# Optimization experiments

Measured on AMD Instinct MI355X. Metric: run time of the kernel, lower is better.

The kernel has to match this reference:

```python
import jax, jax.numpy as jnp
from jax import lax
import numpy as np

B, T, D, H, C = 64, 256, 1024, 1024, 27


def _lstm_layer(x, Wih, Whh, bih, bhh):
    """Batch-first LSTM layer matching torch.nn.LSTM gate math.
    x: (N, S, Din) -> returns hs: (N, S, H). Gate order: i, f, g, o."""
    N = x.shape[0]
    Hh = Whh.shape[1]
    # precompute input contribution for all steps: (N, S, 4H)
    xg = jnp.einsum('nsd,gd->nsg', x, Wih) + bih + bhh

    def step(carry, xg_t):
        h, c = carry
        g = xg_t + h @ Whh.T  # (N, 4H)
        i, f, gg, o = jnp.split(g, 4, axis=-1)
        c = jax.nn.sigmoid(f) * c + jax.nn.sigmoid(i) * jnp.tanh(gg)
        h = jax.nn.sigmoid(o) * jnp.tanh(c)
        return (h, c), h

    h0 = jnp.zeros((N, Hh), x.dtype)
    (_, _), hs = lax.scan(step, (h0, h0), jnp.swapaxes(xg, 0, 1))  # scan over S
    return jnp.swapaxes(hs, 0, 1)  # (N, S, H)


def setup_inputs() -> dict:
    key = jax.random.key(0)
    ks = jax.random.split(key, 13)
    s = 1.0 / np.sqrt(H)
    u = lambda k, shape: jax.random.uniform(k, shape, jnp.float32, -s, s)
    return {
        'x': jax.random.normal(ks[0], (B, T, D), jnp.float32),
        'Wih0': u(ks[1], (4 * H, D)), 'Whh0': u(ks[2], (4 * H, H)),
        'bih0': u(ks[3], (4 * H,)), 'bhh0': u(ks[4], (4 * H,)),
        'Wih1': u(ks[5], (4 * H, H)), 'Whh1': u(ks[6], (4 * H, H)),
        'bih1': u(ks[7], (4 * H,)), 'bhh1': u(ks[8], (4 * H,)),
        'W1': u(ks[9], (H // 2, H)), 'b1': u(ks[10], (H // 2,)),
        'W2': u(ks[11], (C, H // 2)), 'b2': u(ks[12], (C,)),
    }


def reference(x, Wih0, Whh0, bih0, bhh0, Wih1, Whh1, bih1, bhh1, W1, b1, W2, b2):
    # Original module permutes (B,T,D) -> (T,B,D) but the LSTM is batch_first,
    # so it treats T as batch and recurs over the original batch axis B.
    xp = jnp.transpose(x, (1, 0, 2))           # (T, B, D): batch=T, seq=B
    h1 = _lstm_layer(xp, Wih0, Whh0, bih0, bhh0)  # (T, B, H)
    h2 = _lstm_layer(h1, Wih1, Whh1, bih1, bhh1)  # (T, B, H)
    out = h2[-1]                                # (B, H): last 'batch' row
    fc = jax.nn.relu(out @ W1.T + b1)
    return fc @ W2.T + b2                       # (B, C)
```

## Files before the change

kernel.cpp:

```cpp
#include <hip/hip_runtime.h>
#include <math.h>


#define NBLK 256
#define TPB  512
#define HDIM 1024
#define SEQ  64
#define CHAIN (SEQ * HDIM)
#define GUARD (1L << 20)
#define POISON 0xAAAAAAAAu
#define ENCOFF 0x55555555u

#define FMA4(A, W, Hv)                                                         \
  do {                                                                         \
    (A).x = fmaf((W).x, (Hv).x, (A).x);                                        \
    (A).y = fmaf((W).y, (Hv).y, (A).y);                                        \
    (A).z = fmaf((W).z, (Hv).z, (A).z);                                        \
    (A).w = fmaf((W).w, (Hv).w, (A).w);                                        \
  } while (0)

__device__ __forceinline__ float sigmoidf_(float v) {
  return 1.0f / (1.0f + expf(-v));
}
__device__ __forceinline__ float hsum4(float4 a) {
  return (a.x + a.y) + (a.z + a.w);
}
__device__ __forceinline__ float wave_sum(float v) {
#pragma unroll
  for (int m = 32; m >= 1; m >>= 1) v += __shfl_xor(v, m, 64);
  return v;
}

__device__ __forceinline__ void st_u32(unsigned* p, unsigned v) {
  __hip_atomic_store(p, v, __ATOMIC_RELAXED, __HIP_MEMORY_SCOPE_AGENT);
}
__device__ __forceinline__ unsigned enc(float v) {
  return __float_as_uint(v) + ENCOFF;
}
__device__ __forceinline__ float dec(unsigned u) {
  return __uint_as_float(u - ENCOFF);
}
__device__ __forceinline__ float2 poll2(const unsigned* p) {
  const unsigned long long* pp = (const unsigned long long*)p;
  unsigned lo, hi;
  long g = 0;
  for (;;) {
    unsigned long long u =
        __hip_atomic_load(pp, __ATOMIC_RELAXED, __HIP_MEMORY_SCOPE_AGENT);
    lo = (unsigned)u;
    hi = (unsigned)(u >> 32);
    if ((lo != POISON) & (hi != POISON)) break;
    __builtin_amdgcn_s_sleep(1);
    if (++g > GUARD) break;
  }
  asm volatile("" ::: "memory");
  return make_float2(dec(lo), dec(hi));
}

__global__ void __launch_bounds__(TPB, 2) lstm_persist(
    const float* __restrict__ x,
    const float* __restrict__ Wih0, const float* __restrict__ Whh0,
    const float* __restrict__ bih0, const float* __restrict__ bhh0,
    const float* __restrict__ Wih1, const float* __restrict__ Whh1,
    const float* __restrict__ bih1, const float* __restrict__ bhh1,
    const float* __restrict__ W1, const float* __restrict__ b1,
    const float* __restrict__ W2, const float* __restrict__ b2,
    float* __restrict__ out, unsigned* ws, int nrep) {
  __shared__ float sA[2][HDIM];
  __shared__ float sB[2][HDIM];
  __shared__ float sX[2][HDIM];

  unsigned* h1rep = ws;
  unsigned* h2rep = ws + (size_t)nrep * CHAIN;
  unsigned* fcb = ws + 2ull * (size_t)nrep * CHAIN;

  const int tid = threadIdx.x;
  const int b = blockIdx.x;
  const int lane = tid & 63;
  const int q = tid >> 6;
  const int L = q >> 2;
  const int elem = (b << 2) + (q & 3);

  const int rep = b & (nrep - 1);
  unsigned* h1r = h1rep + (size_t)rep * CHAIN;
  unsigned* h2r = h2rep + (size_t)rep * CHAIN;

  const float* Wih = L ? Wih1 : Wih0;
  const float* Whh = L ? Whh1 : Whh0;
  const float* bi = L ? bih1 : bih0;
  const float* bh = L ? bhh1 : bhh0;

  float4 wi[4][4], wr[4][4];
  float bias[4];
#pragma unroll
  for (int g = 0; g < 4; ++g) {
    const int row = (g << 10) + elem;
    bias[g] = bi[row] + bh[row];
    const float4* pi = (const float4*)(Wih + (size_t)row * HDIM);
    const float4* pr = (const float4*)(Whh + (size_t)row * HDIM);
#pragma unroll
    for (int k = 0; k < 4; ++k) {
      wi[g][k] = pi[(k << 6) + lane];
      wr[g][k] = pr[(k << 6) + lane];
    }
  }

  float cell = 0.0f;

  for (int p = 0; p <= SEQ; ++p) {
    const int pb = p & 1;
    float2 xv = make_float2(0, 0);
    if (p < SEQ)
      xv = ((const float2*)x)[(size_t)(p * 256 + 255) * 512 + tid];
    float2 vb = make_float2(0, 0);
    if (p >= 2) vb = poll2(h2r + (size_t)(p - 2) * HDIM + (tid << 1));
    float2 va = make_float2(0, 0);
    if (p >= 1) va = poll2(h1r + (size_t)(p - 1) * HDIM + (tid << 1));

    ((float2*)sA[pb])[tid] = va;
    ((float2*)sB[pb])[tid] = vb;
    ((float2*)sX[pb])[tid] = xv;
    __syncthreads();

    const float4* A4 = (const float4*)sA[pb];
    const float4* B4 = (const float4*)sB[pb];
    const float4* X4 = (const float4*)sX[pb];

    if (L == 0) {
      if (p < SEQ) {
        float4 acc[4];
#pragma unroll
        for (int g = 0; g < 4; ++g) acc[g] = make_float4(0, 0, 0, 0);
#pragma unroll
        for (int k = 0; k < 4; ++k) {
          float4 xf = X4[(k << 6) + lane];
          float4 hf = A4[(k << 6) + lane];
#pragma unroll
          for (int g = 0; g < 4; ++g) {
            FMA4(acc[g], wi[g][k], xf);
            FMA4(acc[g], wr[g][k], hf);
          }
        }
        float gi = wave_sum(hsum4(acc[0])) + bias[0];
        float gf = wave_sum(hsum4(acc[1])) + bias[1];
        float gg = wave_sum(hsum4(acc[2])) + bias[2];
        float go = wave_sum(hsum4(acc[3])) + bias[3];
        cell = sigmoidf_(gf) * cell + sigmoidf_(gi) * tanhf(gg);
        float hv = sigmoidf_(go) * tanhf(cell);
        if (lane < nrep)
          st_u32(h1rep + (size_t)lane * CHAIN + (size_t)p * HDIM + elem,
                 enc(hv));
      }
    } else {
      if (p >= 1) {
        float4 acc[4];
#pragma unroll
        for (int g = 0; g < 4; ++g) acc[g] = make_float4(0, 0, 0, 0);
#pragma unroll
        for (int k = 0; k < 4; ++k) {
          float4 iv = A4[(k << 6) + lane];
          float4 hf = B4[(k << 6) + lane];
#pragma unroll
          for (int g = 0; g < 4; ++g) {
            FMA4(acc[g], wi[g][k], iv);
            FMA4(acc[g], wr[g][k], hf);
          }
        }
        float gi = wave_sum(hsum4(acc[0])) + bias[0];
        float gf = wave_sum(hsum4(acc[1])) + bias[1];
        float gg = wave_sum(hsum4(acc[2])) + bias[2];
        float go = wave_sum(hsum4(acc[3])) + bias[3];
        cell = sigmoidf_(gf) * cell + sigmoidf_(gi) * tanhf(gg);
        float hv = sigmoidf_(go) * tanhf(cell);
        if (lane < nrep)
          st_u32(h2rep + (size_t)lane * CHAIN + (size_t)(p - 1) * HDIM + elem,
                 enc(hv));
      }
    }
  }

  __syncthreads();
  {
    const int s = b >> 2, ch = b & 3;
    float2 v = poll2(h2r + (size_t)s * HDIM + (tid << 1));
    ((float2*)sA[0])[tid] = v;
    __syncthreads();
    const float4* A4 = (const float4*)sA[0];
    for (int t = 0; t < 16; ++t) {
      const int j = (ch << 7) + (q << 4) + t;
      const float4* w4 = (const float4*)(W1 + (size_t)j * HDIM);
      float4 acc = make_float4(0, 0, 0, 0);
#pragma unroll
      for (int k = 0; k < 4; ++k) {
        float4 wv = w4[(k << 6) + lane];
        float4 hv = A4[(k << 6) + lane];
        FMA4(acc, wv, hv);
      }
      float v2 = wave_sum(hsum4(acc));
      if (lane == 0)
        st_u32(fcb + (size_t)s * 512 + j, enc(fmaxf(v2 + b1[j], 0.0f)));
    }
  }

  if (b < 64) {
    if (tid < 256) {
      float2 v = poll2(fcb + (size_t)b * 512 + (tid << 1));
      ((float2*)sB[0])[tid] = v;
    }
    __syncthreads();
    const float4* B4v = (const float4*)sB[0];
    for (int c = q; c < 27; c += 8) {
      const float4* w4 = (const float4*)(W2 + (size_t)c * 512);
      float4 acc = make_float4(0, 0, 0, 0);
#pragma unroll
      for (int k = 0; k < 2; ++k) {
        float4 wv = w4[(k << 6) + lane];
        float4 hv = B4v[(k << 6) + lane];
        FMA4(acc, wv, hv);
      }
      float v = wave_sum(hsum4(acc));
      if (lane == 0) out[b * 27 + c] = v + b2[c];
    }
  }
}

extern "C" void kernel_launch(void* const* d_in, const int* in_sizes, int n_in,
                              void* d_out, int out_size, void* d_ws,
                              size_t ws_size, hipStream_t stream) {
  (void)in_sizes; (void)n_in; (void)out_size;
  const float* x    = (const float*)d_in[0];
  const float* Wih0 = (const float*)d_in[1];
  const float* Whh0 = (const float*)d_in[2];
  const float* bih0 = (const float*)d_in[3];
  const float* bhh0 = (const float*)d_in[4];
  const float* Wih1 = (const float*)d_in[5];
  const float* Whh1 = (const float*)d_in[6];
  const float* bih1 = (const float*)d_in[7];
  const float* bhh1 = (const float*)d_in[8];
  const float* W1   = (const float*)d_in[9];
  const float* b1   = (const float*)d_in[10];
  const float* W2   = (const float*)d_in[11];
  const float* b2   = (const float*)d_in[12];
  float* out = (float*)d_out;
  unsigned* ws = (unsigned*)d_ws;

  int nrep = 1;
  for (int r = 8; r >= 1; r >>= 1) {
    size_t need = (2ull * (size_t)r * CHAIN + (size_t)SEQ * 512) * 4ull;
    if (need <= ws_size) { nrep = r; break; }
  }

  hipLaunchKernelGGL(lstm_persist, dim3(NBLK), dim3(TPB), 0, stream, x, Wih0,
                     Whh0, bih0, bhh0, Wih1, Whh1, bih1, bhh1, W1, b1, W2, b2,
                     out, ws, nrep);
}
```

Baseline: 394.2 us.

## Precompute layer-0 input projection for all steps before the recurrent loop

Layer-0 input gate contributions (Wih0·x + biases) for all 64 timesteps are computed up front in a prologue and kept in shared memory. This removes the per-step x load and the input-matmul FMAs from the layer-0 critical path of the serial recurrence. In exchange it adds a prologue in which each block streams its Wih0 rows and the x rows, and layer-0 warps no longer hold Wih0 in registers.

```diff
diff --git a/kernel.cpp b/kernel.cpp
--- a/kernel.cpp
+++ b/kernel.cpp
@@ -68,7 +68,7 @@
     float* __restrict__ out, unsigned* ws, int nrep) {
   __shared__ float sA[2][HDIM];
   __shared__ float sB[2][HDIM];
-  __shared__ float sX[2][HDIM];
+  __shared__ float xg[16][SEQ];
 
   unsigned* h1rep = ws;
   unsigned* h2rep = ws + (size_t)nrep * CHAIN;
@@ -79,39 +79,62 @@
   const int lane = tid & 63;
   const int q = tid >> 6;
   const int L = q >> 2;
-  const int elem = (b << 2) + (q & 3);
+  const int e = q & 3;
+  const int elem = (b << 2) + e;
 
   const int rep = b & (nrep - 1);
   unsigned* h1r = h1rep + (size_t)rep * CHAIN;
   unsigned* h2r = h2rep + (size_t)rep * CHAIN;
 
-  const float* Wih = L ? Wih1 : Wih0;
-  const float* Whh = L ? Whh1 : Whh0;
-  const float* bi = L ? bih1 : bih0;
-  const float* bh = L ? bhh1 : bhh0;
-
   float4 wi[4][4], wr[4][4];
   float bias[4];
-#pragma unroll
-  for (int g = 0; g < 4; ++g) {
-    const int row = (g << 10) + elem;
-    bias[g] = bi[row] + bh[row];
-    const float4* pi = (const float4*)(Wih + (size_t)row * HDIM);
-    const float4* pr = (const float4*)(Whh + (size_t)row * HDIM);
-#pragma unroll
-    for (int k = 0; k < 4; ++k) {
-      wi[g][k] = pi[(k << 6) + lane];
-      wr[g][k] = pr[(k << 6) + lane];
-    }
-  }
+  if (L == 0) {
+#pragma unroll
+    for (int g = 0; g < 4; ++g) {
+      const int row = (g << 10) + elem;
+      const float4* pr = (const float4*)(Whh0 + (size_t)row * HDIM);
+#pragma unroll
+      for (int k = 0; k < 4; ++k) wr[g][k] = pr[(k << 6) + lane];
+      bias[g] = 0.f;
+    }
+  } else {
+#pragma unroll
+    for (int g = 0; g < 4; ++g) {
+      const int row = (g << 10) + elem;
+      bias[g] = bih1[row] + bhh1[row];
+      const float4* pi = (const float4*)(Wih1 + (size_t)row * HDIM);
+      const float4* pr = (const float4*)(Whh1 + (size_t)row * HDIM);
+#pragma unroll
+      for (int k = 0; k < 4; ++k) {
+        wi[g][k] = pi[(k << 6) + lane];
+        wr[g][k] = pr[(k << 6) + lane];
+      }
+    }
+  }
+
+  for (int r = q; r < 16; r += 8) {
+    const int g = r >> 2, ee = r & 3;
+    const int grow = (g << 10) + (b << 2) + ee;
+    const float4* wrow = (const float4*)(Wih0 + (size_t)grow * HDIM);
+    const float4* xrow =
+        (const float4*)(x + (size_t)(lane * 256 + 255) * HDIM);
+    float4 a0 = make_float4(0.f, 0.f, 0.f, 0.f);
+    float4 a1 = make_float4(0.f, 0.f, 0.f, 0.f);
+#pragma unroll 4
+    for (int kk = 0; kk < 256; kk += 2) {
+      float4 w0 = wrow[kk], x0 = xrow[kk];
+      float4 w1 = wrow[kk + 1], x1 = xrow[kk + 1];
+      FMA4(a0, w0, x0);
+      FMA4(a1, w1, x1);
+    }
+    xg[r][lane] = hsum4(a0) + hsum4(a1) + bih0[grow] + bhh0[grow];
+  }
+  __syncthreads();
 
   float cell = 0.0f;
 
   for (int p = 0; p <= SEQ; ++p) {
     const int pb = p & 1;
-    float2 xv = make_float2(0, 0);
-    if (p < SEQ)
-      xv = ((const float2*)x)[(size_t)(p * 256 + 255) * 512 + tid];
     float2 vb = make_float2(0, 0);
     if (p >= 2) vb = poll2(h2r + (size_t)(p - 2) * HDIM + (tid << 1));
     float2 va = make_float2(0, 0);
@@ -119,12 +142,10 @@
 
     ((float2*)sA[pb])[tid] = va;
     ((float2*)sB[pb])[tid] = vb;
-    ((float2*)sX[pb])[tid] = xv;
     __syncthreads();
 
     const float4* A4 = (const float4*)sA[pb];
     const float4* B4 = (const float4*)sB[pb];
-    const float4* X4 = (const float4*)sX[pb];
 
     if (L == 0) {
       if (p < SEQ) {
@@ -133,18 +154,16 @@
         for (int g = 0; g < 4; ++g) acc[g] = make_float4(0, 0, 0, 0);
 #pragma unroll
         for (int k = 0; k < 4; ++k) {
-          float4 xf = X4[(k << 6) + lane];
           float4 hf = A4[(k << 6) + lane];
 #pragma unroll
           for (int g = 0; g < 4; ++g) {
-            FMA4(acc[g], wi[g][k], xf);
             FMA4(acc[g], wr[g][k], hf);
           }
         }
-        float gi = wave_sum(hsum4(acc[0])) + bias[0];
-        float gf = wave_sum(hsum4(acc[1])) + bias[1];
-        float gg = wave_sum(hsum4(acc[2])) + bias[2];
-        float go = wave_sum(hsum4(acc[3])) + bias[3];
+        float gi = wave_sum(hsum4(acc[0])) + xg[0 * 4 + e][p];
+        float gf = wave_sum(hsum4(acc[1])) + xg[1 * 4 + e][p];
+        float gg = wave_sum(hsum4(acc[2])) + xg[2 * 4 + e][p];
+        float go = wave_sum(hsum4(acc[3])) + xg[3 * 4 + e][p];
         cell = sigmoidf_(gf) * cell + sigmoidf_(gi) * tanhf(gg);
         float hv = sigmoidf_(go) * tanhf(cell);
         if (lane < nrep)
```

New measurement: 547.9 us. +39.0%, slower.
